# Performance work log

Hardware: AMD Instinct MI355X
Metric: run time of the kernel (lower is better)

## Reference

```python
import jax, jax.numpy as jnp
import numpy as np

DIM = 2048
N_HEADS = 16
HEAD_DIM = DIM // N_HEADS  # 128
B, T = 2, 4096
K_CONV = 4
EPS = 1e-5


def _silu(x):
    return x * jax.nn.sigmoid(x)


def _l2norm(x):
    return x * jax.lax.rsqrt(jnp.sum(x * x, axis=-1, keepdims=True) + 1e-6)


def _short_conv(x, w):
    # depthwise causal conv1d, kernel K, then SiLU. x: [B,T,D], w: [D,K]
    K = w.shape[1]
    xp = jnp.pad(x, ((0, 0), (K - 1, 0), (0, 0)))
    y = xp[:, 0:x.shape[1], :] * w[:, 0]
    for i in range(1, K):
        y = y + xp[:, i:i + x.shape[1], :] * w[:, i]
    return _silu(y)


def _delta_rule(q, k, v, beta):
    # DeltaNet recurrence (math-equivalent to fla chunk_delta_rule with
    # use_qk_l2norm_in_kernel=True and default scale Dk**-0.5).
    # q,k: [B,T,H,Dk]; v: [B,T,H,Dv]; beta: [B,T,H]
    Dk = q.shape[-1]
    q = _l2norm(q) * (Dk ** -0.5)
    k = _l2norm(k)
    qT = jnp.swapaxes(q, 0, 1)  # [T,B,H,Dk]
    kT = jnp.swapaxes(k, 0, 1)
    vT = jnp.swapaxes(v, 0, 1)
    bT = jnp.swapaxes(beta, 0, 1)  # [T,B,H]

    def step(S, inp):
        qt, kt, vt, bt = inp
        # prediction error u = v - S^T k
        u = vt - jnp.einsum('bhk,bhkv->bhv', kt, S)
        S = S + bt[:, :, None, None] * kt[..., :, None] * u[..., None, :]
        o = jnp.einsum('bhk,bhkv->bhv', qt, S)
        return S, o

    S0 = jnp.zeros(q.shape[0:1] + q.shape[2:4] + (v.shape[-1],), dtype=q.dtype)
    _, o = jax.lax.scan(step, S0, (qT, kT, vT, bT))
    return jnp.swapaxes(o, 0, 1)  # [B,T,H,Dv]


def _rmsnorm(x, w):
    var = jnp.mean(x * x, axis=-1, keepdims=True)
    return x * jax.lax.rsqrt(var + EPS) * w


def setup_inputs() -> dict:
    key = jax.random.key(0)
    ks = jax.random.split(key, 16)
    std = 0.02
    inp = {
        'hidden_states': jax.random.normal(ks[0], (B, T, DIM), jnp.float32),
        'k_cache': jax.random.normal(ks[1], (B, T, N_HEADS, HEAD_DIM), jnp.float32),
        'v_cache': jax.random.normal(ks[2], (B, T, N_HEADS, HEAD_DIM), jnp.float32),
        'cos': jax.random.normal(ks[3], (B, T, HEAD_DIM), jnp.float32),
        'sin': jax.random.normal(ks[4], (B, T, HEAD_DIM), jnp.float32),
        'Wq': jax.random.normal(ks[5], (DIM, DIM), jnp.float32) * std,
        'Wk': jax.random.normal(ks[6], (DIM, DIM), jnp.float32) * std,
        'Wv': jax.random.normal(ks[7], (DIM, DIM), jnp.float32) * std,
        'Wo': jax.random.normal(ks[8], (DIM, DIM), jnp.float32) * std,
        'Wg': jax.random.normal(ks[9], (DIM, DIM), jnp.float32) * std,
        'Wb': jax.random.normal(ks[10], (DIM, N_HEADS), jnp.float32) * std,
        'conv_wq': jax.random.normal(ks[11], (DIM, K_CONV), jnp.float32) * 0.3,
        'conv_wk': jax.random.normal(ks[12], (DIM, K_CONV), jnp.float32) * 0.3,
        'conv_wv': jax.random.normal(ks[13], (DIM, K_CONV), jnp.float32) * 0.3,
        'norm_w': jnp.ones((HEAD_DIM,), jnp.float32),
    }
    return inp


def reference(hidden_states, k_cache, v_cache, cos, sin,
              Wq, Wk, Wv, Wo, Wg, Wb, conv_wq, conv_wk, conv_wv, norm_w):
    # Deterministic eval path of CrossSwitcher (mode='random', not training,
    # q_len>64): conv -> delta rule -> RMSNorm -> sigmoid gate -> o_proj.
    b, t, d = hidden_states.shape
    q = hidden_states @ Wq
    k = hidden_states @ Wk
    v = hidden_states @ Wv
    q = _short_conv(q, conv_wq)
    k = _short_conv(k, conv_wk)
    v = _short_conv(v, conv_wv)
    q = q.reshape(b, t, N_HEADS, HEAD_DIM)
    k = k.reshape(b, t, N_HEADS, HEAD_DIM)
    v = v.reshape(b, t, N_HEADS, HEAD_DIM)
    beta = jax.nn.sigmoid(hidden_states @ Wb)  # [B,T,H]
    o = _delta_rule(q, k, v, beta)             # [B,T,H,Dh]
    o = _rmsnorm(o, norm_w)
    g = (hidden_states @ Wg).reshape(b, t, N_HEADS, HEAD_DIM)
    o = o * jax.nn.sigmoid(g)
    o = o.reshape(b, t, d) @ Wo
    return o
```

## Files before the change

### kernel.cpp

```cpp
#include <hip/hip_runtime.h>
#include <cstdint>
#include <cstddef>

#define DEVI __device__ __forceinline__

typedef __attribute__((ext_vector_type(8))) short short8;
typedef __attribute__((ext_vector_type(4))) float floatx4;

constexpr int B_ = 2, T_ = 4096, D_ = 2048, H_ = 16, DH = 128;
constexpr int BT = B_ * T_;
constexpr int C_ = 64, NC = T_ / C_;
constexpr int RSQ = 3 * D_;

DEVI float bf2f(ushort u){ union { uint32_t i; float f; } v; v.i = ((uint32_t)u) << 16; return v.f; }
DEVI ushort f2bf(float f){ union { float f; uint32_t i; } v; v.f = f; uint32_t r = v.i + 0x7fff + ((v.i >> 16) & 1); return (ushort)(r >> 16); }
DEVI float sigm(float x){ return 1.f / (1.f + __expf(-x)); }

DEVI void async_load16(const void* g, void* l){
  __builtin_amdgcn_global_load_lds((const __attribute__((address_space(1))) unsigned int*)g,
                                   (__attribute__((address_space(3))) unsigned int*)l, 16, 0, 0);
}
DEVI floatx4 mfma16(short8 a, short8 b, floatx4 c){
  return __builtin_amdgcn_mfma_f32_16x16x32_bf16(a, b, c, 0, 0, 0);
}

__global__ __launch_bounds__(256) void cast_bf16_kernel(const float* __restrict__ x,
                                                        ushort* __restrict__ y, int n){
  int i = (blockIdx.x * 256 + threadIdx.x) * 8;
  if (i + 8 <= n){
    floatx4 a = *(const floatx4*)(x + i);
    floatx4 b = *(const floatx4*)(x + i + 4);
    short8 o;
    o[0]=(short)f2bf(a[0]); o[1]=(short)f2bf(a[1]); o[2]=(short)f2bf(a[2]); o[3]=(short)f2bf(a[3]);
    o[4]=(short)f2bf(b[0]); o[5]=(short)f2bf(b[1]); o[6]=(short)f2bf(b[2]); o[7]=(short)f2bf(b[3]);
    *(short8*)(y + i) = o;
  }
}

__global__ __launch_bounds__(256) void transpose_cast_kernel(const float* __restrict__ w,
                                                             ushort* __restrict__ wt){
  __shared__ float tile[32][33];
  int bx = blockIdx.x, by = blockIdx.y;
  int tx = threadIdx.x & 31, ty = threadIdx.x >> 5;
  #pragma unroll
  for (int j = 0; j < 4; ++j)
    tile[ty + j*8][tx] = w[(size_t)(by*32 + ty + j*8) * D_ + bx*32 + tx];
  __syncthreads();
  #pragma unroll
  for (int j = 0; j < 4; ++j){
    int n = bx*32 + ty + j*8, k = by*32 + tx;
    wt[(size_t)n * D_ + k] = f2bf(tile[tx][ty + j*8]);
  }
}

__global__ __launch_bounds__(256) void cast_wbT(const float* __restrict__ Wb,
                                                ushort* __restrict__ WbT){
  int c = blockIdx.x * 256 + threadIdx.x;
  #pragma unroll
  for (int h = 0; h < H_; ++h)
    WbT[h * D_ + c] = f2bf(Wb[(size_t)c * H_ + h]);
}

#define GSB __builtin_amdgcn_sched_barrier(0)
#define GBAR __builtin_amdgcn_s_barrier()
#define RD_ALO(PA) { _Pragma("unroll") for (int mf = 0; mf < 4; ++mf){ \
    af[mf][0] = frag(PA, wm*128 + mf*16 + l16, 0); \
    af[mf][1] = frag(PA, wm*128 + mf*16 + l16, 1); } }
#define RD_AHI(PA) { _Pragma("unroll") for (int mf = 0; mf < 4; ++mf){ \
    af[mf][0] = frag(PA, wm*128 + (mf+4)*16 + l16, 0); \
    af[mf][1] = frag(PA, wm*128 + (mf+4)*16 + l16, 1); } }
#define RD_B01(PB) { _Pragma("unroll") for (int nf = 0; nf < 2; ++nf){ \
    bf01[nf][0] = frag(PB, wn*64 + nf*16 + l16, 0); \
    bf01[nf][1] = frag(PB, wn*64 + nf*16 + l16, 1); } }
#define RD_B23(PB) { _Pragma("unroll") for (int nf = 0; nf < 2; ++nf){ \
    bf23[nf][0] = frag(PB, wn*64 + (nf+2)*16 + l16, 0); \
    bf23[nf][1] = frag(PB, wn*64 + (nf+2)*16 + l16, 1); } }
#define MFMA_BLK(MO, NO, BF) { _Pragma("unroll") for (int mf = 0; mf < 4; ++mf){ \
    _Pragma("unroll") for (int nf = 0; nf < 2; ++nf){ \
      acc[(MO)+mf][(NO)+nf] = mfma16(af[mf][0], BF[nf][0], acc[(MO)+mf][(NO)+nf]); \
      acc[(MO)+mf][(NO)+nf] = mfma16(af[mf][1], BF[nf][1], acc[(MO)+mf][(NO)+nf]); } } }
#define PH_HEAD GSB; GBAR; GSB; __builtin_amdgcn_s_setprio(1)
#define PH_TAIL __builtin_amdgcn_s_setprio(0)

template<bool F32OUT>
__global__ __launch_bounds__(512) void gemm256k(const ushort* __restrict__ A,
                                                const ushort* __restrict__ Bt,
                                                void* __restrict__ Cv,
                                                int M, int N, int K){
  __shared__ __align__(16) ushort As[2][256 * 64];
  __shared__ __align__(16) ushort Bs[2][256 * 64];
  const int tid = threadIdx.x;
  const int w = tid >> 6, lane = tid & 63, l16 = lane & 15, lq = lane >> 4;
  const int wm = w >> 2, wn = w & 3;
  const int xcd = (int)blockIdx.x & 7, jb = (int)blockIdx.x >> 3;
  const int cpx = gridDim.x >> 3;
  const int ccols = cpx >> 3;
  const int bm = ((xcd & 3) << 3) + (jb & 7);
  const int bn = (xcd >> 2) * ccols + (jb >> 3);
  const int srow = tid >> 3;
  const int ce = ((tid & 7) ^ (srow & 7)) * 8;
  const ushort* Ab = A + (size_t)(bm*256 + srow) * K + ce;
  const ushort* Bb = Bt + (size_t)(bn*256 + srow) * K + ce;
  const int NT = K >> 6;

  floatx4 acc[8][4];
  #pragma unroll
  for (int i = 0; i < 8; ++i)
    #pragma unroll
    for (int jj = 0; jj < 4; ++jj) acc[i][jj] = (floatx4)0.f;

  auto stageA = [&](int kt, int buf){
    #pragma unroll
    for (int jj = 0; jj < 4; ++jj)
      async_load16(Ab + (size_t)(jj*64) * K + kt*64, (char*)&As[buf][0] + (jj*512 + tid)*16);
  };
  auto stageB = [&](int kt, int buf){
    #pragma unroll
    for (int jj = 0; jj < 4; ++jj)
      async_load16(Bb + (size_t)(jj*64) * K + kt*64, (char*)&Bs[buf][0] + (jj*512 + tid)*16);
  };
  auto frag = [&](const ushort* base, int row, int ks) -> short8 {
    int cB = (ks*64 + lq*16) ^ ((row & 7) << 4);
    return *(const short8*)(base + row*64 + (cB >> 1));
  };

  short8 af[4][2], bf01[2][2], bf23[2][2];

  stageA(0, 0); stageB(0, 0);
  stageA(1, 1); stageB(1, 1);
  asm volatile("s_waitcnt vmcnt(8)" ::: "memory");
  GBAR;
  {
    const ushort* pa = &As[0][0]; const ushort* pb = &Bs[0][0];
    RD_ALO(pa); RD_B01(pb); RD_B23(pb);
  }

  #pragma unroll 1
  for (int p = 0; p < NT / 2; ++p){
    const int kt = 2 * p;
    const bool st = (kt + 2 < NT);
    const ushort* pa0 = &As[0][0]; const ushort* pb0 = &Bs[0][0];
    const ushort* pa1 = &As[1][0]; const ushort* pb1 = &Bs[1][0];

    PH_HEAD; MFMA_BLK(0, 0, bf01); PH_TAIL; GSB; GBAR;
    PH_HEAD; MFMA_BLK(0, 2, bf23); PH_TAIL; GSB; GBAR;
    RD_AHI(pa0);
    if (st) stageB(kt + 2, 0);
    PH_HEAD; MFMA_BLK(4, 2, bf23); PH_TAIL;
    if (st) asm volatile("s_waitcnt vmcnt(4)" ::: "memory");
    else    asm volatile("s_waitcnt vmcnt(0)" ::: "memory");
    GSB; GBAR;
    if (st) stageA(kt + 2, 0);
    RD_B23(pb1);
    PH_HEAD; MFMA_BLK(4, 0, bf01); PH_TAIL;
    RD_ALO(pa1); RD_B01(pb1);
    GSB; GBAR;

    PH_HEAD; MFMA_BLK(0, 2, bf23); PH_TAIL; GSB; GBAR;
    PH_HEAD; MFMA_BLK(0, 0, bf01); PH_TAIL; GSB; GBAR;
    RD_AHI(pa1);
    if (st) stageB(kt + 3, 1);
    PH_HEAD; MFMA_BLK(4, 0, bf01); PH_TAIL;
    if (st) asm volatile("s_waitcnt vmcnt(4)" ::: "memory");
    GSB; GBAR;
    if (st){ stageA(kt + 3, 1); RD_B01(pb0); }
    PH_HEAD; MFMA_BLK(4, 2, bf23); PH_TAIL;
    if (st){ RD_ALO(pa0); RD_B23(pb0); }
    GSB; GBAR;
  }

  #pragma unroll
  for (int mf = 0; mf < 8; ++mf)
    #pragma unroll
    for (int nf = 0; nf < 4; ++nf)
      #pragma unroll
      for (int r = 0; r < 4; ++r){
        int row = bm*256 + wm*128 + mf*16 + lq*4 + r;
        int col = bn*256 + wn*64 + nf*16 + l16;
        if (F32OUT) ((float*)Cv)[(size_t)row * N + col] = acc[mf][nf][r];
        else        ((ushort*)Cv)[(size_t)row * N + col] = f2bf(acc[mf][nf][r]);
      }
}

__global__ __launch_bounds__(256) void conv3_kernel(
    const ushort* __restrict__ fqkv,
    const float* __restrict__ cwq, const float* __restrict__ cwk, const float* __restrict__ cwv,
    ushort* __restrict__ qn, ushort* __restrict__ kn, ushort* __restrict__ vc){
  const int blk = blockIdx.x;
  const int b  = (blk * 8) >> 12;
  const int t0 = (blk * 8) & (T_ - 1);
  const int tid = threadIdx.x;
  const int ch0 = tid * 8;

  const float*  cws[3]  = {cwq, cwk, cwv};
  ushort*       dsts[3] = {qn, kn, vc};

  #pragma unroll
  for (int s = 0; s < 3; ++s){
    const ushort* src = fqkv + s * D_;
    floatx4 w[8];
    #pragma unroll
    for (int j = 0; j < 8; ++j) w[j] = *(const floatx4*)&cws[s][(ch0 + j) * 4];

    float xf[11][8];
    #pragma unroll
    for (int idx = 0; idx < 11; ++idx){
      int t = t0 - 3 + idx;
      short8 x = (t >= 0) ? *(const short8*)(src + (size_t)(b*T_ + t)*RSQ + ch0)
                          : (short8)(short)0;
      #pragma unroll
      for (int j = 0; j < 8; ++j) xf[idx][j] = bf2f((ushort)x[j]);
    }

    #pragma unroll
    for (int tt = 0; tt < 8; ++tt){
      float y[8];
      #pragma unroll
      for (int j = 0; j < 8; ++j){
        float a = xf[tt][j]*w[j][0] + xf[tt+1][j]*w[j][1]
                + xf[tt+2][j]*w[j][2] + xf[tt+3][j]*w[j][3];
        y[j] = a * sigm(a);
      }
      float scale = 1.f;
      if (s < 2){
        float ss = 0.f;
        #pragma unroll
        for (int j = 0; j < 8; ++j) ss += y[j]*y[j];
        #pragma unroll
        for (int m = 1; m < 16; m <<= 1) ss += __shfl_xor(ss, m);
        scale = rsqrtf(ss + 1e-6f);
        if (s == 0) scale *= 0.08838834764831845f;
      }
      short8 o;
      #pragma unroll
      for (int j = 0; j < 8; ++j) o[j] = (short)f2bf(y[j] * scale);
      *(short8*)(dsts[s] + (size_t)(b*T_ + t0 + tt)*D_ + ch0) = o;
    }
  }
}

__global__ __launch_bounds__(256) void beta_kernel(const ushort* __restrict__ hb,
                                                   const ushort* __restrict__ WbT,
                                                   float* __restrict__ beta){
  const int r = blockIdx.x * 4 + (threadIdx.x >> 6);
  const int lane = threadIdx.x & 63;
  float xf[32];
  #pragma unroll
  for (int i = 0; i < 4; ++i){
    short8 x = *(const short8*)(hb + (size_t)r * D_ + i*512 + lane*8);
    #pragma unroll
    for (int j = 0; j < 8; ++j) xf[i*8 + j] = bf2f((ushort)x[j]);
  }
  float res = 0.f;
  #pragma unroll
  for (int h = 0; h < H_; ++h){
    float s = 0.f;
    #pragma unroll
    for (int i = 0; i < 4; ++i){
      short8 wv = *(const short8*)(WbT + (size_t)h * D_ + i*512 + lane*8);
      #pragma unroll
      for (int j = 0; j < 8; ++j) s += xf[i*8 + j] * bf2f((ushort)wv[j]);
    }
    #pragma unroll
    for (int m = 1; m < 64; m <<= 1) s += __shfl_xor(s, m);
    if (lane == h) res = s;
  }
  if (lane < H_) beta[(size_t)r * H_ + lane] = sigm(res);
}

__global__ __launch_bounds__(256) void phase1(
    const ushort* __restrict__ kn, const ushort* __restrict__ vc, const float* __restrict__ beta,
    ushort* __restrict__ Wneg, ushort* __restrict__ U, ushort* __restrict__ KTg){
  __shared__ __align__(16) char smem[72960];
  ushort* Ks = (ushort*)smem;
  ushort* Xb = (ushort*)smem;
  ushort* KT = (ushort*)(smem + 17408);
  ushort* VT = (ushort*)(smem + 17408 + 18432);
  ushort* Xt = (ushort*)(smem + 17408 + 36864);
  ushort* Pb = (ushort*)(smem + 17408 + 36864 + 9216);
  float*  bet = (float*)(smem + 17408 + 36864 + 18432);

  const int bx = blockIdx.x;
  const int c = bx & 63, h = (bx >> 6) & 15, b = bx >> 10;
  const int t0 = c * 64;
  const int tid = threadIdx.x, w = tid >> 6, lane = tid & 63, l16 = lane & 15, lq = lane >> 4;

  {
    int i = tid >> 2, d0 = (tid & 3) * 32;
    const ushort* kp = kn + (size_t)(b*T_ + t0 + i) * D_ + h*DH + d0;
    const ushort* vp = vc + (size_t)(b*T_ + t0 + i) * D_ + h*DH + d0;
    #pragma unroll
    for (int j = 0; j < 4; ++j){
      short8 kv = *(const short8*)(kp + j*8);
      short8 vv = *(const short8*)(vp + j*8);
      *(short8*)&Ks[i*136 + d0 + j*8] = kv;
      #pragma unroll
      for (int e = 0; e < 8; ++e){
        int d = d0 + j*8 + e;
        KT[d*72 + i] = (ushort)kv[e];
        VT[d*72 + i] = (ushort)vv[e];
      }
    }
    if (tid < 64) bet[tid] = beta[(size_t)(b*T_ + t0 + tid) * H_ + h];
  }
  __syncthreads();

  floatx4 accL[4];
  #pragma unroll
  for (int fn = 0; fn < 4; ++fn) accL[fn] = (floatx4)0.f;
  #pragma unroll
  for (int ks = 0; ks < 4; ++ks){
    short8 a = *(const short8*)&Ks[(w*16 + l16)*136 + ks*32 + lq*8];
    #pragma unroll
    for (int fn = 0; fn < 4; ++fn){
      short8 bb = *(const short8*)&Ks[(fn*16 + l16)*136 + ks*32 + lq*8];
      accL[fn] = mfma16(a, bb, accL[fn]);
    }
  }
  __syncthreads();

  {
    size_t kb = (size_t)bx * (128 * 64);
    int d = tid >> 1, i0 = (tid & 1) * 32;
    #pragma unroll
    for (int j = 0; j < 4; ++j)
      *(short8*)(KTg + kb + d*64 + i0 + j*8) = *(const short8*)&KT[d*72 + i0 + j*8];
  }

  #pragma unroll
  for (int fn = 0; fn < 4; ++fn)
    #pragma unroll
    for (int r = 0; r < 4; ++r){
      int i = w*16 + lq*4 + r, j = fn*16 + l16;
      float v = (j < i) ? (-bet[i] * accL[fn][r]) : 0.f;
      ushort vb = f2bf(v);
      Xb[i*72 + j] = vb;
      Xt[j*72 + i] = vb;
      Pb[i*72 + j] = (i == j) ? f2bf(1.f) : vb;
    }
  __syncthreads();

  #pragma unroll 1
  for (int s = 0; s < 5; ++s){
    floatx4 accY[4];
    #pragma unroll
    for (int fn = 0; fn < 4; ++fn) accY[fn] = (floatx4)0.f;
    #pragma unroll
    for (int ks = 0; ks < 2; ++ks){
      short8 a = *(const short8*)&Xb[(w*16 + l16)*72 + ks*32 + lq*8];
      #pragma unroll
      for (int fn = 0; fn < 4; ++fn){
        short8 bb = *(const short8*)&Xt[(fn*16 + l16)*72 + ks*32 + lq*8];
        accY[fn] = mfma16(a, bb, accY[fn]);
      }
    }
    __syncthreads();
    #pragma unroll
    for (int fn = 0; fn < 4; ++fn)
      #pragma unroll
      for (int r = 0; r < 4; ++r){
        int i = w*16 + lq*4 + r, n = fn*16 + l16;
        ushort v = f2bf(accY[fn][r]);
        Xb[i*72 + n] = v;
        Xt[n*72 + i] = v;
      }
    __syncthreads();
    floatx4 accP[4];
    #pragma unroll
    for (int fn = 0; fn < 4; ++fn)
      #pragma unroll
      for (int r = 0; r < 4; ++r)
        accP[fn][r] = bf2f(Pb[(w*16 + lq*4 + r)*72 + fn*16 + l16]);
    #pragma unroll
    for (int ks = 0; ks < 2; ++ks){
      short8 a = *(const short8*)&Pb[(w*16 + l16)*72 + ks*32 + lq*8];
      #pragma unroll
      for (int fn = 0; fn < 4; ++fn){
        short8 bb = *(const short8*)&Xt[(fn*16 + l16)*72 + ks*32 + lq*8];
        accP[fn] = mfma16(a, bb, accP[fn]);
      }
    }
    #pragma unroll
    for (int fn = 0; fn < 4; ++fn)
      #pragma unroll
      for (int r = 0; r < 4; ++r)
        Pb[(w*16 + lq*4 + r)*72 + fn*16 + l16] = f2bf(accP[fn][r]);
    __syncthreads();
  }

  floatx4 accW[8], accU[8];
  #pragma unroll
  for (int fn = 0; fn < 8; ++fn){ accW[fn] = (floatx4)0.f; accU[fn] = (floatx4)0.f; }
  #pragma unroll
  for (int ks = 0; ks < 2; ++ks){
    short8 p = *(const short8*)&Pb[(w*16 + l16)*72 + ks*32 + lq*8];
    short8 a;
    #pragma unroll
    for (int e = 0; e < 8; ++e)
      a[e] = (short)f2bf(bf2f((ushort)p[e]) * bet[ks*32 + lq*8 + e]);
    #pragma unroll
    for (int fn = 0; fn < 8; ++fn){
      short8 bk = *(const short8*)&KT[(fn*16 + l16)*72 + ks*32 + lq*8];
      short8 bv = *(const short8*)&VT[(fn*16 + l16)*72 + ks*32 + lq*8];
      accW[fn] = mfma16(a, bk, accW[fn]);
      accU[fn] = mfma16(a, bv, accU[fn]);
    }
  }
  size_t base = (size_t)bx * (64 * 128);
  #pragma unroll
  for (int fn = 0; fn < 8; ++fn)
    #pragma unroll
    for (int r = 0; r < 4; ++r){
      int i = w*16 + lq*4 + r, d = fn*16 + l16;
      Wneg[base + i*128 + d] = f2bf(-accW[fn][r]);
      U[base + i*128 + d]    = f2bf(accU[fn][r]);
    }
}

__global__ __launch_bounds__(256) void phase2(
    const ushort* __restrict__ qn, const ushort* __restrict__ KTg,
    const ushort* __restrict__ Wneg, const ushort* __restrict__ U,
    ushort* __restrict__ UpT, ushort* __restrict__ Opart){
  __shared__ __align__(16) ushort Sb[32 * 136];
  __shared__ __align__(16) ushort Ws[64 * 136];
  __shared__ __align__(16) ushort Qs[64 * 136];
  __shared__ __align__(16) ushort KTc[128 * 72];
  __shared__ __align__(16) ushort Us[64 * 40];
  __shared__ __align__(16) ushort UT[32 * 72];

  const int bx = blockIdx.x;
  const int xcd = bx & 7, j = bx >> 3;
  const int bh = xcd * 4 + (j >> 2), vs = j & 3;
  const int b = bh >> 4, h = bh & 15;
  const int tid = threadIdx.x, w = tid >> 6, lane = tid & 63, l16 = lane & 15, lq = lane >> 4;

  for (int e = tid; e < 32*136; e += 256) Sb[e] = 0;

  floatx4 M[2][2];
  #pragma unroll
  for (int nf = 0; nf < 2; ++nf)
    #pragma unroll
    for (int kf = 0; kf < 2; ++kf) M[nf][kf] = (floatx4)0.f;

  const int si = tid >> 2, sd = (tid & 3) * 32;
  short8 rW[4], rQ[4], rK[4], rU;

  auto loadr = [&](int c){
    size_t cb = ((size_t)(bh*NC + c)) * (64 * 128);
    const ushort* wp = Wneg + cb + si*128 + sd;
    const ushort* qp = qn + ((size_t)(b*T_ + c*64 + si)) * D_ + h*DH + sd;
    const ushort* kp = KTg + cb + tid*32;
    #pragma unroll
    for (int j2 = 0; j2 < 4; ++j2){
      rW[j2] = *(const short8*)(wp + j2*8);
      rQ[j2] = *(const short8*)(qp + j2*8);
      rK[j2] = *(const short8*)(kp + j2*8);
    }
    rU = *(const short8*)(U + cb + si*128 + vs*32 + (tid & 3)*8);
  };
  loadr(0);

  for (int c = 0; c < NC; ++c){
    #pragma unroll
    for (int j2 = 0; j2 < 4; ++j2){
      *(short8*)&Ws[si*136 + sd + j2*8] = rW[j2];
      *(short8*)&Qs[si*136 + sd + j2*8] = rQ[j2];
      *(short8*)&KTc[(tid >> 1)*72 + (tid & 1)*32 + j2*8] = rK[j2];
    }
    *(short8*)&Us[si*40 + (tid & 3)*8] = rU;
    __syncthreads();
    if (c + 1 < NC) loadr(c + 1);

    floatx4 accU[2];
    #pragma unroll
    for (int fn = 0; fn < 2; ++fn)
      #pragma unroll
      for (int r = 0; r < 4; ++r)
        accU[fn][r] = bf2f(Us[(w*16 + lq*4 + r)*40 + fn*16 + l16]);
    #pragma unroll
    for (int ks = 0; ks < 4; ++ks){
      short8 a = *(const short8*)&Ws[(w*16 + l16)*136 + ks*32 + lq*8];
      #pragma unroll
      for (int fn = 0; fn < 2; ++fn){
        short8 bs = *(const short8*)&Sb[(fn*16 + l16)*136 + ks*32 + lq*8];
        accU[fn] = mfma16(a, bs, accU[fn]);
      }
    }
    #pragma unroll
    for (int fn = 0; fn < 2; ++fn)
      #pragma unroll
      for (int r = 0; r < 4; ++r)
        UT[(fn*16 + l16)*72 + w*16 + lq*4 + r] = f2bf(accU[fn][r]);
    __syncthreads();

    size_t cb = ((size_t)(bh*NC + c)) * (64 * 128);
    {
      int nl = tid >> 3, i0 = (tid & 7) * 8;
      *(short8*)(UpT + cb + (size_t)(vs*32 + nl)*64 + i0) = *(const short8*)&UT[nl*72 + i0];
    }
    floatx4 accO[2];
    #pragma unroll
    for (int fn = 0; fn < 2; ++fn) accO[fn] = (floatx4)0.f;
    #pragma unroll
    for (int ks = 0; ks < 4; ++ks){
      short8 a = *(const short8*)&Qs[(w*16 + l16)*136 + ks*32 + lq*8];
      #pragma unroll
      for (int fn = 0; fn < 2; ++fn){
        short8 bs = *(const short8*)&Sb[(fn*16 + l16)*136 + ks*32 + lq*8];
        accO[fn] = mfma16(a, bs, accO[fn]);
      }
    }
    #pragma unroll
    for (int fn = 0; fn < 2; ++fn)
      #pragma unroll
      for (int r = 0; r < 4; ++r){
        int i = w*16 + lq*4 + r;
        Opart[cb + (size_t)i*128 + vs*32 + fn*16 + l16] = f2bf(accO[fn][r]);
      }
    #pragma unroll
    for (int ks = 0; ks < 2; ++ks){
      short8 a0 = *(const short8*)&UT[(l16)*72 + ks*32 + lq*8];
      short8 a1 = *(const short8*)&UT[(16 + l16)*72 + ks*32 + lq*8];
      #pragma unroll
      for (int kf = 0; kf < 2; ++kf){
        short8 bk = *(const short8*)&KTc[(w*32 + kf*16 + l16)*72 + ks*32 + lq*8];
        M[0][kf] = mfma16(a0, bk, M[0][kf]);
        M[1][kf] = mfma16(a1, bk, M[1][kf]);
      }
    }
    __syncthreads();
    #pragma unroll
    for (int nf = 0; nf < 2; ++nf)
      #pragma unroll
      for (int kf = 0; kf < 2; ++kf)
        #pragma unroll
        for (int r = 0; r < 4; ++r)
          Sb[(nf*16 + lq*4 + r)*136 + w*32 + kf*16 + l16] = f2bf(M[nf][kf][r]);
  }
}

__global__ __launch_bounds__(256) void phase3(
    const ushort* __restrict__ qn, const ushort* __restrict__ kn,
    const ushort* __restrict__ UpT, const ushort* __restrict__ Opart,
    const ushort* g, const float* __restrict__ norm_w,
    ushort* og){
  __shared__ __align__(16) ushort Qs[64 * 136];
  __shared__ __align__(16) ushort Ks[64 * 136];
  __shared__ __align__(16) ushort UTs[128 * 72];
  __shared__ __align__(16) ushort Os[64 * 136];
  __shared__ __align__(16) ushort Gs[64 * 136];
  __shared__ __align__(16) ushort Ab[64 * 72];
  __shared__ float nw[128];

  const int bx = blockIdx.x;
  const int c = bx & 63, h = (bx >> 6) & 15, b = bx >> 10;
  const int t0 = c * 64;
  const int tid = threadIdx.x, w = tid >> 6, lane = tid & 63, l16 = lane & 15, lq = lane >> 4;
  const size_t cb = (size_t)bx * (64 * 128);

  {
    int i = tid >> 2, d0 = (tid & 3) * 32;
    const ushort* qp = qn + (size_t)(b*T_ + t0 + i) * D_ + h*DH + d0;
    const ushort* kp = kn + (size_t)(b*T_ + t0 + i) * D_ + h*DH + d0;
    const ushort* gp = g  + (size_t)(b*T_ + t0 + i) * D_ + h*DH + d0;
    const ushort* op = Opart + cb + i*128 + d0;
    #pragma unroll
    for (int j = 0; j < 4; ++j){
      *(short8*)&Qs[i*136 + d0 + j*8] = *(const short8*)(qp + j*8);
      *(short8*)&Ks[i*136 + d0 + j*8] = *(const short8*)(kp + j*8);
      *(short8*)&Gs[i*136 + d0 + j*8] = *(const short8*)(gp + j*8);
      *(short8*)&Os[i*136 + d0 + j*8] = *(const short8*)(op + j*8);
    }
    int n = tid >> 1, i0 = (tid & 1) * 32;
    #pragma unroll
    for (int j = 0; j < 4; ++j)
      *(short8*)&UTs[n*72 + i0 + j*8] = *(const short8*)(UpT + cb + n*64 + i0 + j*8);
    if (tid < 128) nw[tid] = norm_w[tid];
  }
  __syncthreads();

  floatx4 accA[4];
  #pragma unroll
  for (int fn = 0; fn < 4; ++fn) accA[fn] = (floatx4)0.f;
  #pragma unroll
  for (int ks = 0; ks < 4; ++ks){
    short8 a = *(const short8*)&Qs[(w*16 + l16)*136 + ks*32 + lq*8];
    #pragma unroll
    for (int fn = 0; fn < 4; ++fn){
      short8 bb = *(const short8*)&Ks[(fn*16 + l16)*136 + ks*32 + lq*8];
      accA[fn] = mfma16(a, bb, accA[fn]);
    }
  }
  #pragma unroll
  for (int fn = 0; fn < 4; ++fn)
    #pragma unroll
    for (int r = 0; r < 4; ++r){
      int i = w*16 + lq*4 + r, j = fn*16 + l16;
      Ab[i*72 + j] = f2bf((j <= i) ? accA[fn][r] : 0.f);
    }
  __syncthreads();

  floatx4 accO[8];
  #pragma unroll
  for (int fn = 0; fn < 8; ++fn)
    #pragma unroll
    for (int r = 0; r < 4; ++r)
      accO[fn][r] = bf2f(Os[(w*16 + lq*4 + r)*136 + fn*16 + l16]);
  #pragma unroll
  for (int ks = 0; ks < 2; ++ks){
    short8 a = *(const short8*)&Ab[(w*16 + l16)*72 + ks*32 + lq*8];
    #pragma unroll
    for (int fn = 0; fn < 8; ++fn){
      short8 bu = *(const short8*)&UTs[(fn*16 + l16)*72 + ks*32 + lq*8];
      accO[fn] = mfma16(a, bu, accO[fn]);
    }
  }
  #pragma unroll
  for (int r = 0; r < 4; ++r){
    float ss = 0.f;
    #pragma unroll
    for (int fn = 0; fn < 8; ++fn) ss += accO[fn][r] * accO[fn][r];
    #pragma unroll
    for (int m = 1; m < 16; m <<= 1) ss += __shfl_xor(ss, m);
    float rms = rsqrtf(ss * (1.f / 128.f) + 1e-5f);
    int i = w*16 + lq*4 + r;
    #pragma unroll
    for (int fn = 0; fn < 8; ++fn){
      int d = fn*16 + l16;
      float gv = bf2f(Gs[i*136 + d]);
      float o = accO[fn][r] * rms * nw[d] * sigm(gv);
      og[(size_t)(b*T_ + t0 + i) * D_ + h*DH + d] = f2bf(o);
    }
  }
}

extern "C" void kernel_launch(void* const* d_in, const int* in_sizes, int n_in,
                              void* d_out, int out_size, void* d_ws, size_t ws_size,
                              hipStream_t stream){
  const float* hidden = (const float*)d_in[0];
  const float* Wq = (const float*)d_in[5];
  const float* Wk = (const float*)d_in[6];
  const float* Wv = (const float*)d_in[7];
  const float* Wo = (const float*)d_in[8];
  const float* Wg = (const float*)d_in[9];
  const float* Wb = (const float*)d_in[10];
  const float* cwq = (const float*)d_in[11];
  const float* cwk = (const float*)d_in[12];
  const float* cwv = (const float*)d_in[13];
  const float* nw  = (const float*)d_in[14];

  char* ws = (char*)d_ws;
  size_t off = 0;
  auto alloc = [&](size_t bytes){ void* p = ws + off; off += (bytes + 255) & ~(size_t)255; return p; };
  const size_t SZ = (size_t)BT * D_ * 2;
  ushort* hb   = (ushort*)alloc(SZ);
  ushort* wqT  = (ushort*)alloc((size_t)D_*D_*2);
  ushort* wkT  = (ushort*)alloc((size_t)D_*D_*2);
  ushort* wvT  = (ushort*)alloc((size_t)D_*D_*2);
  ushort* wgT  = (ushort*)alloc((size_t)D_*D_*2);
  ushort* woT  = (ushort*)alloc((size_t)D_*D_*2);
  ushort* wbT  = (ushort*)alloc((size_t)H_*D_*2);
  ushort* fqkv = (ushort*)alloc(3*SZ);
  ushort* kn   = (ushort*)alloc(SZ);
  ushort* vcv  = (ushort*)alloc(SZ);
  float*  beta = (float*)alloc((size_t)BT * H_ * 4);
  (void)in_sizes; (void)n_in; (void)out_size;
  if (off > ws_size) return;

  ushort* qn  = (ushort*)d_out;
  ushort* KTg = (ushort*)d_out + (size_t)BT * D_;

  cast_bf16_kernel<<<8192, 256, 0, stream>>>(hidden, hb, BT * D_);
  dim3 tg(64, 64);
  transpose_cast_kernel<<<tg, 256, 0, stream>>>(Wq, wqT);
  transpose_cast_kernel<<<tg, 256, 0, stream>>>(Wk, wkT);
  transpose_cast_kernel<<<tg, 256, 0, stream>>>(Wv, wvT);
  transpose_cast_kernel<<<tg, 256, 0, stream>>>(Wg, wgT);
  transpose_cast_kernel<<<tg, 256, 0, stream>>>(Wo, woT);
  cast_wbT<<<D_/256, 256, 0, stream>>>(Wb, wbT);

  {
    const int NWG = (BT / 256) * (RSQ / 256);
    gemm256k<false><<<NWG, 512, 0, stream>>>(hb, wqT, fqkv, BT, RSQ, D_);
  }

  conv3_kernel<<<BT/8, 256, 0, stream>>>(fqkv, cwq, cwk, cwv, qn, kn, vcv);
  beta_kernel<<<BT/4, 256, 0, stream>>>(hb, wbT, beta);

  ushort* gpre = fqkv;
  ushort* Wneg = fqkv + (size_t)BT * D_;
  ushort* Ubuf = fqkv + (size_t)2 * BT * D_;
  {
    const int NWG = (BT / 256) * (D_ / 256);
    gemm256k<false><<<NWG, 512, 0, stream>>>(hb, wgT, gpre, BT, D_, D_);
  }

  ushort* Opart = hb;

  phase1<<<B_ * H_ * NC, 256, 0, stream>>>(kn, vcv, beta, Wneg, Ubuf, KTg);
  ushort* UpT = vcv;
  phase2<<<B_ * H_ * 4, 256, 0, stream>>>(qn, KTg, Wneg, Ubuf, UpT, Opart);
  ushort* og = gpre;
  phase3<<<B_ * H_ * NC, 256, 0, stream>>>(qn, kn, UpT, Opart, gpre, nw, og);

  {
    const int NWG = (BT / 256) * (D_ / 256);
    gemm256k<true><<<NWG, 512, 0, stream>>>(og, woT, (float*)d_out, BT, D_, D_);
  }
}
```

Before: 732.8 us.

## Parallelize delta-rule state recurrence across segments with affine segment scan

Splits the sequential chunk recurrence in phase2 into 8 segments. A new seg kernel computes each segment's affine state transform: an offset from a zero start and a linear part from an identity start. A small scan kernel composes these transforms sequentially to get each segment's starting state. Phase2 then runs 1024 blocks instead of 128, each starting from its precomputed state. This exposes more parallelism on the serial critical path, at the cost of extra matmul work, two more launches and added bf16 rounding error in the composed states.

Measured after the change: 786.0 us. 7.3% more time.

```diff
diff --git a/kernel.cpp b/kernel.cpp
--- a/kernel.cpp
+++ b/kernel.cpp
@@ -11,6 +11,7 @@
 constexpr int BT = B_ * T_;
 constexpr int C_ = 64, NC = T_ / C_;
 constexpr int RSQ = 3 * D_;
+constexpr int NSEG = 8, SEGC = NC / NSEG;
 
 DEVI float bf2f(ushort u){ union { uint32_t i; float f; } v; v.i = ((uint32_t)u) << 16; return v.f; }
 DEVI ushort f2bf(float f){ union { float f; uint32_t i; } v; v.f = f; uint32_t r = v.i + 0x7fff + ((v.i >> 16) & 1); return (ushort)(r >> 16); }
@@ -417,9 +418,199 @@
     }
 }
 
+__global__ __launch_bounds__(256) void seg_kernel(
+    const ushort* __restrict__ KTg, const ushort* __restrict__ Wneg,
+    const ushort* __restrict__ U, ushort* __restrict__ SegB, ushort* __restrict__ SegA){
+  __shared__ __align__(16) ushort Sb[32 * 136];
+  __shared__ __align__(16) ushort Ws[64 * 136];
+  __shared__ __align__(16) ushort KTc[128 * 72];
+  __shared__ __align__(16) ushort Us[64 * 40];
+  __shared__ __align__(16) ushort UT[32 * 72];
+
+  const int bx = blockIdx.x;
+  const int part = bx >> 10;
+  const int b2 = bx & 1023;
+  const int vs = b2 & 3, seg = (b2 >> 2) & 7, bh = b2 >> 5;
+  const int tid = threadIdx.x, w = tid >> 6, lane = tid & 63, l16 = lane & 15, lq = lane >> 4;
+
+  floatx4 M[2][2];
+  if (part == 0){
+    #pragma unroll
+    for (int nf = 0; nf < 2; ++nf)
+      #pragma unroll
+      for (int kf = 0; kf < 2; ++kf) M[nf][kf] = (floatx4)0.f;
+    for (int e = tid; e < 32*136; e += 256) Sb[e] = 0;
+  } else {
+    #pragma unroll
+    for (int nf = 0; nf < 2; ++nf)
+      #pragma unroll
+      for (int kf = 0; kf < 2; ++kf)
+        #pragma unroll
+        for (int r = 0; r < 4; ++r){
+          int n = vs*32 + nf*16 + lq*4 + r;
+          int k = w*32 + kf*16 + l16;
+          M[nf][kf][r] = (n == k) ? 1.f : 0.f;
+        }
+    #pragma unroll
+    for (int nf = 0; nf < 2; ++nf)
+      #pragma unroll
+      for (int kf = 0; kf < 2; ++kf)
+        #pragma unroll
+        for (int r = 0; r < 4; ++r)
+          Sb[(nf*16 + lq*4 + r)*136 + w*32 + kf*16 + l16] = f2bf(M[nf][kf][r]);
+  }
+
+  const int si = tid >> 2, sd = (tid & 3) * 32;
+  short8 rW[4], rK[4], rU;
+  auto loadr = [&](int c){
+    size_t cb = ((size_t)(bh*NC + seg*SEGC + c)) * (64 * 128);
+    const ushort* wp = Wneg + cb + si*128 + sd;
+    const ushort* kp = KTg + cb + tid*32;
+    #pragma unroll
+    for (int j2 = 0; j2 < 4; ++j2){
+      rW[j2] = *(const short8*)(wp + j2*8);
+      rK[j2] = *(const short8*)(kp + j2*8);
+    }
+    if (part == 0) rU = *(const short8*)(U + cb + si*128 + vs*32 + (tid & 3)*8);
+  };
+  loadr(0);
+
+  for (int c = 0; c < SEGC; ++c){
+    #pragma unroll
+    for (int j2 = 0; j2 < 4; ++j2){
+      *(short8*)&Ws[si*136 + sd + j2*8] = rW[j2];
+      *(short8*)&KTc[(tid >> 1)*72 + (tid & 1)*32 + j2*8] = rK[j2];
+    }
+    if (part == 0) *(short8*)&Us[si*40 + (tid & 3)*8] = rU;
+    __syncthreads();
+    if (c + 1 < SEGC) loadr(c + 1);
+
+    floatx4 accU[2];
+    #pragma unroll
+    for (int fn = 0; fn < 2; ++fn)
+      #pragma unroll
+      for (int r = 0; r < 4; ++r)
+        accU[fn][r] = (part == 0) ? bf2f(Us[(w*16 + lq*4 + r)*40 + fn*16 + l16]) : 0.f;
+    #pragma unroll
+    for (int ks = 0; ks < 4; ++ks){
+      short8 a = *(const short8*)&Ws[(w*16 + l16)*136 + ks*32 + lq*8];
+      #pragma unroll
+      for (int fn = 0; fn < 2; ++fn){
+        short8 bs = *(const short8*)&Sb[(fn*16 + l16)*136 + ks*32 + lq*8];
+        accU[fn] = mfma16(a, bs, accU[fn]);
+      }
+    }
+    #pragma unroll
+    for (int fn = 0; fn < 2; ++fn)
+      #pragma unroll
+      for (int r = 0; r < 4; ++r)
+        UT[(fn*16 + l16)*72 + w*16 + lq*4 + r] = f2bf(accU[fn][r]);
+    __syncthreads();
+
+    #pragma unroll
+    for (int ks = 0; ks < 2; ++ks){
+      short8 a0 = *(const short8*)&UT[(l16)*72 + ks*32 + lq*8];
+      short8 a1 = *(const short8*)&UT[(16 + l16)*72 + ks*32 + lq*8];
+      #pragma unroll
+      for (int kf = 0; kf < 2; ++kf){
+        short8 bk = *(const short8*)&KTc[(w*32 + kf*16 + l16)*72 + ks*32 + lq*8];
+        M[0][kf] = mfma16(a0, bk, M[0][kf]);
+        M[1][kf] = mfma16(a1, bk, M[1][kf]);
+      }
+    }
+    __syncthreads();
+    #pragma unroll
+    for (int nf = 0; nf < 2; ++nf)
+      #pragma unroll
+      for (int kf = 0; kf < 2; ++kf)
+        #pragma unroll
+        for (int r = 0; r < 4; ++r)
+          Sb[(nf*16 + lq*4 + r)*136 + w*32 + kf*16 + l16] = f2bf(M[nf][kf][r]);
+  }
+
+  ushort* dst = (part ? SegA : SegB) + ((size_t)(bh*NSEG + seg)) * (128 * 128);
+  #pragma unroll
+  for (int nf = 0; nf < 2; ++nf)
+    #pragma unroll
+    for (int kf = 0; kf < 2; ++kf)
+      #pragma unroll
+      for (int r = 0; r < 4; ++r)
+        dst[(size_t)(vs*32 + nf*16 + lq*4 + r)*128 + w*32 + kf*16 + l16] = f2bf(M[nf][kf][r]);
+}
+
+__global__ __launch_bounds__(256) void scan_kernel(const ushort* __restrict__ SegA,
+                                                   ushort* __restrict__ SegB){
+  __shared__ __align__(16) ushort Sb[32 * 136];
+  __shared__ __align__(16) ushort AN[128 * 136];
+  const int bx = blockIdx.x;
+  const int vs = bx & 3, bh = bx >> 2;
+  const int tid = threadIdx.x, w = tid >> 6, lane = tid & 63, l16 = lane & 15, lq = lane >> 4;
+
+  floatx4 M[2][2];
+  #pragma unroll
+  for (int nf = 0; nf < 2; ++nf)
+    #pragma unroll
+    for (int kf = 0; kf < 2; ++kf) M[nf][kf] = (floatx4)0.f;
+  for (int e = tid; e < 32*136; e += 256) Sb[e] = 0;
+
+  for (int s = 0; s < NSEG; ++s){
+    const ushort* Ap = SegA + ((size_t)(bh*NSEG + s)) * (128 * 128);
+    {
+      int a = tid >> 1, h0 = (tid & 1) * 64;
+      #pragma unroll
+      for (int jj = 0; jj < 8; ++jj){
+        short8 kv = *(const short8*)(Ap + (size_t)a*128 + h0 + jj*8);
+        #pragma unroll
+        for (int e = 0; e < 8; ++e) AN[(h0 + jj*8 + e)*136 + a] = (ushort)kv[e];
+      }
+    }
+    __syncthreads();
+
+    const ushort* Bp = SegB + ((size_t)(bh*NSEG + s)) * (128 * 128);
+    floatx4 nM[2][2];
+    #pragma unroll
+    for (int nf = 0; nf < 2; ++nf)
+      #pragma unroll
+      for (int kf = 0; kf < 2; ++kf)
+        #pragma unroll
+        for (int r = 0; r < 4; ++r)
+          nM[nf][kf][r] = bf2f(Bp[(size_t)(vs*32 + nf*16 + lq*4 + r)*128 + w*32 + kf*16 + l16]);
+    #pragma unroll
+    for (int ks = 0; ks < 4; ++ks){
+      short8 a0 = *(const short8*)&Sb[(l16)*136 + ks*32 + lq*8];
+      short8 a1 = *(const short8*)&Sb[(16 + l16)*136 + ks*32 + lq*8];
+      #pragma unroll
+      for (int kf = 0; kf < 2; ++kf){
+        short8 bk = *(const short8*)&AN[(w*32 + kf*16 + l16)*136 + ks*32 + lq*8];
+        nM[0][kf] = mfma16(a0, bk, nM[0][kf]);
+        nM[1][kf] = mfma16(a1, bk, nM[1][kf]);
+      }
+    }
+    __syncthreads();
+    #pragma unroll
+    for (int nf = 0; nf < 2; ++nf)
+      #pragma unroll
+      for (int kf = 0; kf < 2; ++kf){
+        M[nf][kf] = nM[nf][kf];
+        #pragma unroll
+        for (int r = 0; r < 4; ++r)
+          Sb[(nf*16 + lq*4 + r)*136 + w*32 + kf*16 + l16] = f2bf(M[nf][kf][r]);
+      }
+    ushort* Pout = SegB + ((size_t)(bh*NSEG + s)) * (128 * 128);
+    #pragma unroll
+    for (int nf = 0; nf < 2; ++nf)
+      #pragma unroll
+      for (int kf = 0; kf < 2; ++kf)
+        #pragma unroll
+        for (int r = 0; r < 4; ++r)
+          Pout[(size_t)(vs*32 + nf*16 + lq*4 + r)*128 + w*32 + kf*16 + l16] = f2bf(M[nf][kf][r]);
+  }
+}
+
 __global__ __launch_bounds__(256) void phase2(
     const ushort* __restrict__ qn, const ushort* __restrict__ KTg,
     const ushort* __restrict__ Wneg, const ushort* __restrict__ U,
+    const ushort* __restrict__ SegS,
     ushort* __restrict__ UpT, ushort* __restrict__ Opart){
   __shared__ __align__(16) ushort Sb[32 * 136];
   __shared__ __align__(16) ushort Ws[64 * 136];
@@ -429,26 +620,36 @@
   __shared__ __align__(16) ushort UT[32 * 72];
 
   const int bx = blockIdx.x;
-  const int xcd = bx & 7, j = bx >> 3;
-  const int bh = xcd * 4 + (j >> 2), vs = j & 3;
+  const int vs = bx & 3, seg = (bx >> 2) & 7, bh = bx >> 5;
   const int b = bh >> 4, h = bh & 15;
   const int tid = threadIdx.x, w = tid >> 6, lane = tid & 63, l16 = lane & 15, lq = lane >> 4;
 
-  for (int e = tid; e < 32*136; e += 256) Sb[e] = 0;
-
   floatx4 M[2][2];
-  #pragma unroll
-  for (int nf = 0; nf < 2; ++nf)
-    #pragma unroll
-    for (int kf = 0; kf < 2; ++kf) M[nf][kf] = (floatx4)0.f;
+  if (seg == 0){
+    #pragma unroll
+    for (int nf = 0; nf < 2; ++nf)
+      #pragma unroll
+      for (int kf = 0; kf < 2; ++kf) M[nf][kf] = (floatx4)0.f;
+    for (int e = tid; e < 32*136; e += 256) Sb[e] = 0;
+  } else {
+    const ushort* s0 = SegS + ((size_t)(bh*NSEG + seg - 1)) * (128 * 128);
+    #pragma unroll
+    for (int nf = 0; nf < 2; ++nf)
+      #pragma unroll
+      for (int kf = 0; kf < 2; ++kf)
+        #pragma unroll
+        for (int r = 0; r < 4; ++r){
+          M[nf][kf][r] = bf2f(s0[(size_t)(vs*32 + nf*16 + lq*4 + r)*128 + w*32 + kf*16 + l16]);
+          Sb[(nf*16 + lq*4 + r)*136 + w*32 + kf*16 + l16] = f2bf(M[nf][kf][r]);
+        }
+  }
 
   const int si = tid >> 2, sd = (tid & 3) * 32;
   short8 rW[4], rQ[4], rK[4], rU;
-
   auto loadr = [&](int c){
-    size_t cb = ((size_t)(bh*NC + c)) * (64 * 128);
+    size_t cb = ((size_t)(bh*NC + seg*SEGC + c)) * (64 * 128);
     const ushort* wp = Wneg + cb + si*128 + sd;
-    const ushort* qp = qn + ((size_t)(b*T_ + c*64 + si)) * D_ + h*DH + sd;
+    const ushort* qp = qn + ((size_t)(b*T_ + (seg*SEGC + c)*64 + si)) * D_ + h*DH + sd;
     const ushort* kp = KTg + cb + tid*32;
     #pragma unroll
     for (int j2 = 0; j2 < 4; ++j2){
@@ -460,7 +661,7 @@
   };
   loadr(0);
 
-  for (int c = 0; c < NC; ++c){
+  for (int c = 0; c < SEGC; ++c){
     #pragma unroll
     for (int j2 = 0; j2 < 4; ++j2){
       *(short8*)&Ws[si*136 + sd + j2*8] = rW[j2];
@@ -469,7 +670,7 @@
     }
     *(short8*)&Us[si*40 + (tid & 3)*8] = rU;
     __syncthreads();
-    if (c + 1 < NC) loadr(c + 1);
+    if (c + 1 < SEGC) loadr(c + 1);
 
     floatx4 accU[2];
     #pragma unroll
@@ -493,7 +694,7 @@
         UT[(fn*16 + l16)*72 + w*16 + lq*4 + r] = f2bf(accU[fn][r]);
     __syncthreads();
 
-    size_t cb = ((size_t)(bh*NC + c)) * (64 * 128);
+    size_t cb = ((size_t)(bh*NC + seg*SEGC + c)) * (64 * 128);
     {
       int nl = tid >> 3, i0 = (tid & 7) * 8;
       *(short8*)(UpT + cb + (size_t)(vs*32 + nl)*64 + i0) = *(const short8*)&UT[nl*72 + i0];
@@ -664,6 +865,8 @@
   ushort* kn   = (ushort*)alloc(SZ);
   ushort* vcv  = (ushort*)alloc(SZ);
   float*  beta = (float*)alloc((size_t)BT * H_ * 4);
+  ushort* segB = (ushort*)alloc((size_t)32*NSEG*128*128*2);
+  ushort* segA = (ushort*)alloc((size_t)32*NSEG*128*128*2);
   (void)in_sizes; (void)n_in; (void)out_size;
   if (off > ws_size) return;
 
@@ -698,8 +901,11 @@
   ushort* Opart = hb;
 
   phase1<<<B_ * H_ * NC, 256, 0, stream>>>(kn, vcv, beta, Wneg, Ubuf, KTg);
+
+  seg_kernel<<<2048, 256, 0, stream>>>(KTg, Wneg, Ubuf, segB, segA);
+  scan_kernel<<<128, 256, 0, stream>>>(segA, segB);
   ushort* UpT = vcv;
-  phase2<<<B_ * H_ * 4, 256, 0, stream>>>(qn, KTg, Wneg, Ubuf, UpT, Opart);
+  phase2<<<1024, 256, 0, stream>>>(qn, KTg, Wneg, Ubuf, segB, UpT, Opart);
   ushort* og = gpre;
   phase3<<<B_ * H_ * NC, 256, 0, stream>>>(qn, kn, UpT, Opart, gpre, nw, og);
 
```
